# Performance work log

Hardware: AMD Instinct MI355X
Metric: run time of the kernel (lower is better)

Reference implementation:

```python
import jax, jax.numpy as jnp
import numpy as np

DECAY = 0.999
EPS = 1e-05


def setup_inputs() -> dict:
    key = jax.random.key(0)
    k1, k2 = jax.random.split(key)
    B, L, S, D, E = 32, 8, 512, 256, 2048
    x = jax.random.normal(k1, (B, L, S, D), dtype=jnp.float32)
    # stacked per-quantizer codebooks: embed[l] is the [dim, n_embed] buffer of Quantize l
    embed = jax.random.normal(k2, (L, D, E), dtype=jnp.float32)
    cluster_size = jnp.zeros((L, E), dtype=jnp.float32)
    embed_avg = embed.copy()
    return {"x": x, "embed": embed, "cluster_size": cluster_size, "embed_avg": embed_avg}


def reference(x, embed, cluster_size, embed_avg):
    # x: [B, L, S, D]; embed: [L, D, E]; cluster_size: [L, E]; embed_avg: [L, D, E]
    B, L, S, D = x.shape
    E = embed.shape[-1]

    dist = ((x * x).sum(-1, keepdims=True)
            - 2.0 * jnp.einsum('blsd,lde->blse', x, embed)
            + (embed * embed).sum(1)[None, :, None, :])
    ids = jnp.argmin(dist, axis=-1)  # argmax of -dist == argmin of dist; [B, L, S]

    # codebook lookup: embed_t[l, ids[b,l,s]] -> [B, L, S, D]
    embed_t = jnp.swapaxes(embed, 1, 2)  # [L, E, D]
    q = embed_t[jnp.arange(L)[None, :, None], ids]

    # EMA buffer updates (training mode; done on .data in torch, i.e. no grad)
    l_idx = jnp.broadcast_to(jnp.arange(L)[None, :, None], (B, L, S))
    counts = jnp.zeros((L, E), x.dtype).at[l_idx, ids].add(1.0)  # onehot.sum(0) per quantizer
    embed_sum = jnp.zeros((L, E, D), x.dtype).at[l_idx, ids].add(jax.lax.stop_gradient(x))
    embed_sum = jnp.swapaxes(embed_sum, 1, 2)  # [L, D, E] == flatten.T @ onehot
    new_cluster_size = DECAY * cluster_size + (1.0 - DECAY) * counts
    new_embed_avg = DECAY * embed_avg + (1.0 - DECAY) * embed_sum
    n = new_cluster_size.sum(-1, keepdims=True)  # [L, 1]
    cs = (new_cluster_size + EPS) / (n + E * EPS) * n
    new_embed = new_embed_avg / cs[:, None, :]

    # NOTE: the original loop overwrites `diff` each iteration then does `diff += diff`,
    # so the returned diff is 2 * diff_of_last_quantizer / length (faithfully reproduced).
    diff_last = jnp.mean((jax.lax.stop_gradient(q[:, L - 1]) - x[:, L - 1]) ** 2)
    diff = 2.0 * diff_last / L

    # straight-through estimator
    out = x + jax.lax.stop_gradient(q - x)
    return out, diff, ids, new_embed, new_cluster_size, new_embed_avg
```

## Files before the change

kernel.cpp:

```cpp
#include <hip/hip_runtime.h>

#define LL 8
#define BB 32
#define SS 512
#define DD 256
#define EE 2048
#define LED (LL*DD*EE)
#define LE  (LL*EE)
#define NROWS (BB*LL*SS)
#define NSEG 32

typedef __bf16 bf16x8 __attribute__((ext_vector_type(8)));
typedef float  f32x16 __attribute__((ext_vector_type(16)));

__global__ void prep_transpose_kernel(const float* __restrict__ embed,
                                      float* __restrict__ embed_t,
                                      float* __restrict__ norms,
                                      __bf16* __restrict__ frag) {
    __shared__ float tile[32][33];
    const int l  = blockIdx.z;
    const int d0 = blockIdx.y * 32;
    const int e0 = blockIdx.x * 32;
    const int tx = threadIdx.x, ty = threadIdx.y;

    float v = embed[((size_t)l*DD + d0 + ty)*EE + e0 + tx];
    tile[ty][tx] = v;
    __syncthreads();

    embed_t[((size_t)l*EE + e0 + ty)*DD + d0 + tx] = tile[tx][ty];

    const int t    = ty*32 + tx;
    const int ksl  = t >> 9;
    const int pos  = t & 511;
    const int lane = pos >> 3, j = pos & 7;
    const int klocal = (lane >> 5)*8 + j;
    const int e_loc  = lane & 31;
    float val = tile[ksl*16 + klocal][e_loc];
    __bf16 h = (__bf16)val;
    const int m  = blockIdx.x;
    const int ks = (d0 >> 4) + ksl;
    size_t segbase = (((size_t)(l*64 + m))*NSEG + 2*ks)*512 + pos;
    frag[segbase]       = h;
    frag[segbase + 512] = (__bf16)(val - (float)h);

    if (ty == 0) {
        float s = 0.f;
        #pragma unroll
        for (int i = 0; i < 32; ++i) s += tile[i][tx]*tile[i][tx];
        atomicAdd(&norms[l*EE + e0 + tx], s);
    }
}

__global__ __launch_bounds__(256, 2)
void argmin_mfma(const float* __restrict__ x,
                 const __bf16* __restrict__ frag,
                 const float* __restrict__ embed_t,
                 const float* __restrict__ norms,
                 int* __restrict__ ids_out,
                 int* __restrict__ counts_i,
                 float* __restrict__ out,
                 float* __restrict__ diff_acc) {
    __shared__ __bf16 slots[2][NSEG*512];
    __shared__ float  normbuf[EE];

    const int tid  = threadIdx.x;
    const int wave = tid >> 6, lane = tid & 63;
    const int l    = blockIdx.x & 7;
    const int rb   = blockIdx.x >> 3;
    const int idx  = rb*4 + wave;
    const int b    = idx >> 4, st = idx & 15;
    const int rowtile = (b*LL + l)*16 + st;

    {
        const float* np = norms + l*EE;
        for (int i = wave; i < 8; i += 4) {
            __builtin_amdgcn_global_load_lds(
                (const __attribute__((address_space(1))) void*)(np + i*256 + lane*4),
                (__attribute__((address_space(3))) void*)(normbuf + i*256), 16, 0, 0);
        }
    }

    bf16x8 bh[16], bl[16];
    {
        const float* xr = x + (size_t)(rowtile*32 + (lane & 31))*DD + (lane >> 5)*8;
        #pragma unroll
        for (int ks = 0; ks < 16; ++ks) {
            float4 v0 = *(const float4*)(xr + ks*16);
            float4 v1 = *(const float4*)(xr + ks*16 + 4);
            float f[8] = {v0.x, v0.y, v0.z, v0.w, v1.x, v1.y, v1.z, v1.w};
            #pragma unroll
            for (int j = 0; j < 8; ++j) {
                __bf16 h = (__bf16)f[j];
                bh[ks][j] = h;
                bl[ks][j] = (__bf16)(f[j] - (float)h);
            }
        }
    }

    const __bf16* fl = frag + (size_t)l*64*NSEG*512;

    auto stage = [&](int m, int buf) {
        const __bf16* src = fl + (size_t)m*NSEG*512 + lane*8;
        __bf16* dst = &slots[buf][0];
        for (int i = wave; i < NSEG; i += 4) {
            __builtin_amdgcn_global_load_lds(
                (const __attribute__((address_space(1))) void*)(src + i*512),
                (__attribute__((address_space(3))) void*)(dst + i*512), 16, 0, 0);
        }
    };

    float maxv = -3.4e38f;
    int   maxi = 0;

    stage(0, 0);
    __syncthreads();

    #pragma unroll 1
    for (int m = 0; m < 64; ++m) {
        const int buf = m & 1;
        if (m < 63) stage(m + 1, buf ^ 1);

        f32x16 a0, a1, a2;
        #pragma unroll
        for (int i = 0; i < 16; ++i) { a0[i] = 0.0f; a1[i] = 0.0f; a2[i] = 0.0f; }

        const __bf16* sA = &slots[buf][0];
        __builtin_amdgcn_s_setprio(1);
        #pragma unroll
        for (int k = 0; k < 16; ++k) {
            bf16x8 ah = *(const bf16x8*)(sA + (2*k    )*512 + lane*8);
            bf16x8 al = *(const bf16x8*)(sA + (2*k + 1)*512 + lane*8);
            a0 = __builtin_amdgcn_mfma_f32_32x32x16_bf16(ah, bh[k], a0, 0, 0, 0);
            a1 = __builtin_amdgcn_mfma_f32_32x32x16_bf16(ah, bl[k], a1, 0, 0, 0);
            a2 = __builtin_amdgcn_mfma_f32_32x32x16_bf16(al, bh[k], a2, 0, 0, 0);
        }
        __builtin_amdgcn_s_setprio(0);

        const int ebase = m*32 + 4*(lane >> 5);
        #pragma unroll
        for (int j = 0; j < 4; ++j) {
            float4 nv = *(const float4*)(normbuf + m*32 + 8*j + 4*(lane >> 5));
            #pragma unroll
            for (int rr = 0; rr < 4; ++rr) {
                float v = a0[4*j + rr] + a1[4*j + rr] + a2[4*j + rr];
                v = fmaf(-0.5f, (&nv.x)[rr], v);
                int e = ebase + rr + 8*j;
                if (v > maxv) { maxv = v; maxi = e; }
            }
        }
        __syncthreads();
    }

    float ov = __shfl_xor(maxv, 32, 64);
    int   oi = __shfl_xor(maxi, 32, 64);
    if (ov > maxv || (ov == maxv && oi < maxi)) { maxv = ov; maxi = oi; }
    if (lane < 32) {
        ids_out[(size_t)rowtile*32 + lane] = maxi;
        atomicAdd(&counts_i[l*EE + maxi], 1);
    }

    const float4* et4  = (const float4*)embed_t;
    const float4* x4   = (const float4*)x;
    float4*       out4 = (float4*)out;
    float sq = 0.f;
    #pragma unroll 4
    for (int r = 0; r < 32; ++r) {
        int id = __shfl(maxi, r);
        float4 qv = et4[((size_t)l*EE + id)*64 + lane];
        size_t o = ((size_t)rowtile*32 + r)*64 + lane;
        out4[o] = qv;
        if (l == LL - 1) {
            float4 xv = x4[o];
            float dx = qv.x - xv.x, dy = qv.y - xv.y, dz = qv.z - xv.z, dw = qv.w - xv.w;
            sq += dx*dx + dy*dy + dz*dz + dw*dw;
        }
    }
    if (l == LL - 1) {
        #pragma unroll
        for (int off = 32; off; off >>= 1) sq += __shfl_down(sq, off);
        if (lane == 0) atomicAdd(diff_acc, sq);
    }
}

__global__ __launch_bounds__(256)
void scan_kernel(const int* __restrict__ counts_i,
                 const float* __restrict__ cs_in,
                 int* __restrict__ bin_start,
                 int* __restrict__ cursor,
                 float* __restrict__ ncs_out,
                 float* __restrict__ n_out) {
    __shared__ int part[256];
    __shared__ float red[4];
    const int l = blockIdx.x, tid = threadIdx.x;
    const int base = l*EE + tid*8;
    int local[8], tsum = 0;
    float fsum = 0.f;
    #pragma unroll
    for (int j = 0; j < 8; ++j) {
        local[j] = counts_i[base + j];
        tsum += local[j];
        float v = 0.999f*cs_in[base + j] + 0.001f*(float)local[j];
        ncs_out[base + j] = v;
        fsum += v;
    }
    part[tid] = tsum;
    __syncthreads();
    for (int off = 1; off < 256; off <<= 1) {
        int v = (tid >= off) ? part[tid - off] : 0;
        __syncthreads();
        part[tid] += v;
        __syncthreads();
    }
    int run = part[tid] - tsum;
    #pragma unroll
    for (int j = 0; j < 8; ++j) {
        bin_start[base + j] = run;
        cursor[base + j]    = run;
        run += local[j];
    }
    #pragma unroll
    for (int off = 32; off; off >>= 1) fsum += __shfl_down(fsum, off);
    if ((tid & 63) == 0) red[tid >> 6] = fsum;
    __syncthreads();
    if (tid == 0) n_out[l] = red[0] + red[1] + red[2] + red[3];
}

__global__ __launch_bounds__(256)
void scatter_idx_kernel(const int* __restrict__ ids,
                        int* __restrict__ cursor,
                        int* __restrict__ sorted_rows) {
    const int r = blockIdx.x*256 + threadIdx.x;
    const int l = (r >> 9) & 7;
    const int e = ids[r];
    int pos = atomicAdd(&cursor[l*EE + e], 1);
    sorted_rows[l*(NROWS/LL) + pos] = r;
}

__global__ __launch_bounds__(256)
void segsum_kernel(const float* __restrict__ x,
                   const int* __restrict__ sorted_rows,
                   const int* __restrict__ bin_start,
                   const int* __restrict__ counts_i,
                   float* __restrict__ embed_sum) {
    const int bid = blockIdx.x;
    const int l   = bid >> 11;
    const int e   = bid & 2047;
    const int tid = threadIdx.x;
    const int start = bin_start[l*EE + e];
    const int cnt   = counts_i[l*EE + e];
    const int* rows = sorted_rows + l*(NROWS/LL);

    float acc = 0.f;
    int i = 0;
    for (; i + 1 < cnt; i += 2) {
        int r0 = rows[start + i], r1 = rows[start + i + 1];
        acc += x[(size_t)r0*DD + tid] + x[(size_t)r1*DD + tid];
    }
    if (i < cnt) acc += x[(size_t)rows[start + i]*DD + tid];
    embed_sum[((size_t)l*EE + e)*DD + tid] = acc;
}

__global__ void finalize_embed_kernel(const float* __restrict__ embed_avg,
                                      const float* __restrict__ embed_sum,
                                      const float* __restrict__ ncs,
                                      const float* __restrict__ n,
                                      float* __restrict__ nea_out,
                                      float* __restrict__ ne_out) {
    __shared__ float tile[32][33];
    const int l  = blockIdx.z;
    const int d0 = blockIdx.y * 32;
    const int e0 = blockIdx.x * 32;
    const int tx = threadIdx.x, ty = threadIdx.y;

    tile[ty][tx] = embed_sum[((size_t)l*EE + e0 + ty)*DD + d0 + tx];
    __syncthreads();
    const size_t idx = ((size_t)l*DD + d0 + ty)*EE + e0 + tx;
    float nea = 0.999f*embed_avg[idx] + 0.001f*tile[tx][ty];
    nea_out[idx] = nea;
    float nl = n[l];
    float c  = ncs[l*EE + e0 + tx];
    float cs = (c + 1e-5f) / (nl + 0.02048f) * nl;
    ne_out[idx] = nea / cs;
}

__global__ void diff_scale_kernel(const float* __restrict__ diff_acc,
                                  float* __restrict__ diff_out) {
    *diff_out = (*diff_acc / (float)(BB*SS*DD)) * 0.25f;
}

extern "C" void kernel_launch(void* const* d_in, const int* in_sizes, int n_in,
                              void* d_out, int out_size, void* d_ws, size_t ws_size,
                              hipStream_t stream) {
    const float* x            = (const float*)d_in[0];
    const float* embed        = (const float*)d_in[1];
    const float* cluster_size = (const float*)d_in[2];
    const float* embed_avg    = (const float*)d_in[3];

    float* out      = (float*)d_out;
    float* diff_out = out + 33554432;
    int*   ids_out  = (int*)(out + 33554433);
    float* ne_out   = out + 33685505;
    float* ncs_out  = out + 37879809;
    float* nea_out  = out + 37896193;

    float* ws        = (float*)d_ws;
    float* embed_t   = ws;
    float* embed_sum = ws + LED;
    int*   counts_i  = (int*)(ws + 2*(size_t)LED);
    float* norms     = ws + 2*(size_t)LED + LE;
    float* diff_acc  = norms + LE;
    float* n_ws      = diff_acc + 1;
    int*   bin_start = (int*)(n_ws + LL);
    int*   cursor    = bin_start + LE;
    int*   sorted_rows = cursor + LE;
    __bf16* embfrag  = (__bf16*)(sorted_rows + NROWS + 16);

    hipMemsetAsync(counts_i, 0, (size_t)(2*LE + 1) * sizeof(float), stream);

    prep_transpose_kernel<<<dim3(EE/32, DD/32, LL), dim3(32, 32), 0, stream>>>(
        embed, embed_t, norms, embfrag);

    argmin_mfma<<<1024, 256, 0, stream>>>(x, embfrag, embed_t, norms, ids_out,
                                          counts_i, out, diff_acc);

    scan_kernel<<<LL, 256, 0, stream>>>(counts_i, cluster_size, bin_start, cursor,
                                        ncs_out, n_ws);

    scatter_idx_kernel<<<NROWS/256, 256, 0, stream>>>(ids_out, cursor, sorted_rows);

    segsum_kernel<<<LE, 256, 0, stream>>>(x, sorted_rows, bin_start, counts_i, embed_sum);

    finalize_embed_kernel<<<dim3(EE/32, DD/32, LL), dim3(32, 32), 0, stream>>>(
        embed_avg, embed_sum, ncs_out, n_ws, nea_out, ne_out);

    diff_scale_kernel<<<1, 1, 0, stream>>>(diff_acc, diff_out);
}
```

Before: 959.7 us.

## Fold codebook norms into MFMA and software-pipeline argmin epilogue

Adds a 33rd fragment segment holding -0.5*|e|^2 split into bf16 hi/lo, paired with a constant-ones B fragment, so the norm bias is accumulated by one extra MFMA instead of a separate LDS norm buffer and FMA. The main loop is restructured to ping-pong accumulators so the argmin compare for the previous codebook tile is interleaved with the current tile's MFMAs, using sched_group_barrier hints and register prefetch of A fragments. Accumulators are merged from three to two. It adds a small kernel launch and extra LDS and register pressure, and the bf16 split of the norm may change rounding slightly.

```diff
diff --git a/kernel.cpp b/kernel.cpp
--- a/kernel.cpp
+++ b/kernel.cpp
@@ -8,7 +8,7 @@
 #define LED (LL*DD*EE)
 #define LE  (LL*EE)
 #define NROWS (BB*LL*SS)
-#define NSEG 32
+#define NSEG 33
 
 typedef __bf16 bf16x8 __attribute__((ext_vector_type(8)));
 typedef float  f32x16 __attribute__((ext_vector_type(16)));
@@ -51,17 +51,31 @@
     }
 }
 
+__global__ void norm_seg_kernel(const float* __restrict__ norms,
+                                __bf16* __restrict__ frag) {
+    const int bid  = blockIdx.x;
+    const int lane = threadIdx.x;
+    bf16x8 v;
+    #pragma unroll
+    for (int j = 0; j < 8; ++j) v[j] = (__bf16)0.0f;
+    if (lane < 32) {
+        float nv = -0.5f * norms[(bid >> 6)*EE + (bid & 63)*32 + lane];
+        __bf16 h = (__bf16)nv;
+        v[0] = h;
+        v[1] = (__bf16)(nv - (float)h);
+    }
+    *(bf16x8*)(frag + ((size_t)bid*NSEG + 32)*512 + lane*8) = v;
+}
+
 __global__ __launch_bounds__(256, 2)
 void argmin_mfma(const float* __restrict__ x,
                  const __bf16* __restrict__ frag,
                  const float* __restrict__ embed_t,
-                 const float* __restrict__ norms,
                  int* __restrict__ ids_out,
                  int* __restrict__ counts_i,
                  float* __restrict__ out,
                  float* __restrict__ diff_acc) {
     __shared__ __bf16 slots[2][NSEG*512];
-    __shared__ float  normbuf[EE];
 
     const int tid  = threadIdx.x;
     const int wave = tid >> 6, lane = tid & 63;
@@ -71,16 +85,7 @@
     const int b    = idx >> 4, st = idx & 15;
     const int rowtile = (b*LL + l)*16 + st;
 
-    {
-        const float* np = norms + l*EE;
-        for (int i = wave; i < 8; i += 4) {
-            __builtin_amdgcn_global_load_lds(
-                (const __attribute__((address_space(1))) void*)(np + i*256 + lane*4),
-                (__attribute__((address_space(3))) void*)(normbuf + i*256), 16, 0, 0);
-        }
-    }
-
-    bf16x8 bh[16], bl[16];
+    bf16x8 bh[17], bl[16];
     {
         const float* xr = x + (size_t)(rowtile*32 + (lane & 31))*DD + (lane >> 5)*8;
         #pragma unroll
@@ -95,6 +100,9 @@
                 bl[ks][j] = (__bf16)(f[j] - (float)h);
             }
         }
+        #pragma unroll
+        for (int j = 0; j < 8; ++j) bh[16][j] = (__bf16)0.0f;
+        if (lane < 32) { bh[16][0] = (__bf16)1.0f; bh[16][1] = (__bf16)1.0f; }
     }
 
     const __bf16* fl = frag + (size_t)l*64*NSEG*512;
@@ -109,46 +117,66 @@
         }
     };
 
-    float maxv = -3.4e38f;
+    float maxv = -1e30f;
     int   maxi = 0;
 
-    stage(0, 0);
-    __syncthreads();
-
-    #pragma unroll 1
-    for (int m = 0; m < 64; ++m) {
-        const int buf = m & 1;
-        if (m < 63) stage(m + 1, buf ^ 1);
-
-        f32x16 a0, a1, a2;
-        #pragma unroll
-        for (int i = 0; i < 16; ++i) { a0[i] = 0.0f; a1[i] = 0.0f; a2[i] = 0.0f; }
-
-        const __bf16* sA = &slots[buf][0];
-        __builtin_amdgcn_s_setprio(1);
+    auto step = [&](int m, f32x16& Pc, f32x16& Qc, f32x16& Pp, f32x16& Qp) {
+        #pragma unroll
+        for (int i = 0; i < 16; ++i) { Pc[i] = 0.0f; Qc[i] = 0.0f; }
+        if (m < 63) stage(m + 1, (m & 1) ^ 1);
+        const __bf16* sA = &slots[m & 1][0];
+        const int pbase = (m - 1)*32 + 4*(lane >> 5);
+
+        bf16x8 ah = *(const bf16x8*)(sA + 0*512 + lane*8);
+        bf16x8 al = *(const bf16x8*)(sA + 1*512 + lane*8);
         #pragma unroll
         for (int k = 0; k < 16; ++k) {
-            bf16x8 ah = *(const bf16x8*)(sA + (2*k    )*512 + lane*8);
-            bf16x8 al = *(const bf16x8*)(sA + (2*k + 1)*512 + lane*8);
-            a0 = __builtin_amdgcn_mfma_f32_32x32x16_bf16(ah, bh[k], a0, 0, 0, 0);
-            a1 = __builtin_amdgcn_mfma_f32_32x32x16_bf16(ah, bl[k], a1, 0, 0, 0);
-            a2 = __builtin_amdgcn_mfma_f32_32x32x16_bf16(al, bh[k], a2, 0, 0, 0);
-        }
-        __builtin_amdgcn_s_setprio(0);
-
-        const int ebase = m*32 + 4*(lane >> 5);
-        #pragma unroll
-        for (int j = 0; j < 4; ++j) {
-            float4 nv = *(const float4*)(normbuf + m*32 + 8*j + 4*(lane >> 5));
-            #pragma unroll
-            for (int rr = 0; rr < 4; ++rr) {
-                float v = a0[4*j + rr] + a1[4*j + rr] + a2[4*j + rr];
-                v = fmaf(-0.5f, (&nv.x)[rr], v);
-                int e = ebase + rr + 8*j;
+            bf16x8 nh, nl;
+            if (k < 15) {
+                nh = *(const bf16x8*)(sA + (2*k + 2)*512 + lane*8);
+                nl = *(const bf16x8*)(sA + (2*k + 3)*512 + lane*8);
+            } else {
+                nh = *(const bf16x8*)(sA + 32*512 + lane*8);
+                nl = nh;
+            }
+            Pc = __builtin_amdgcn_mfma_f32_32x32x16_bf16(ah, bh[k], Pc, 0, 0, 0);
+            Qc = __builtin_amdgcn_mfma_f32_32x32x16_bf16(ah, bl[k], Qc, 0, 0, 0);
+            Pc = __builtin_amdgcn_mfma_f32_32x32x16_bf16(al, bh[k], Pc, 0, 0, 0);
+            {
+                float v = Pp[k] + Qp[k];
+                int e = pbase + (k & 3) + 8*(k >> 2);
                 if (v > maxv) { maxv = v; maxi = e; }
             }
-        }
+            ah = nh; al = nl;
+            if (k < 15) __builtin_amdgcn_sched_group_barrier(0x100, 2, 0);
+            else        __builtin_amdgcn_sched_group_barrier(0x100, 1, 0);
+            __builtin_amdgcn_sched_group_barrier(0x008, 3, 0);
+            __builtin_amdgcn_sched_group_barrier(0x002, 8, 0);
+        }
+        Pc = __builtin_amdgcn_mfma_f32_32x32x16_bf16(ah, bh[16], Pc, 0, 0, 0);
         __syncthreads();
+    };
+
+    f32x16 PA, QA, PB, QB;
+    #pragma unroll
+    for (int i = 0; i < 16; ++i) { PB[i] = -1e30f; QB[i] = -1e30f; }
+
+    stage(0, 0);
+    __syncthreads();
+
+    #pragma unroll 1
+    for (int t = 0; t < 32; ++t) {
+        step(2*t,     PA, QA, PB, QB);
+        step(2*t + 1, PB, QB, PA, QA);
+    }
+    {
+        const int pbase = 63*32 + 4*(lane >> 5);
+        #pragma unroll
+        for (int k = 0; k < 16; ++k) {
+            float v = PB[k] + QB[k];
+            int e = pbase + (k & 3) + 8*(k >> 2);
+            if (v > maxv) { maxv = v; maxi = e; }
+        }
     }
 
     float ov = __shfl_xor(maxv, 32, 64);
@@ -320,7 +348,9 @@
     prep_transpose_kernel<<<dim3(EE/32, DD/32, LL), dim3(32, 32), 0, stream>>>(
         embed, embed_t, norms, embfrag);
 
-    argmin_mfma<<<1024, 256, 0, stream>>>(x, embfrag, embed_t, norms, ids_out,
+    norm_seg_kernel<<<LL*64, 64, 0, stream>>>(norms, embfrag);
+
+    argmin_mfma<<<1024, 256, 0, stream>>>(x, embfrag, embed_t, ids_out,
                                           counts_i, out, diff_acc);
 
     scan_kernel<<<LL, 256, 0, stream>>>(counts_i, cluster_size, bin_start, cursor,
```

Measured after the change: 945.0 us. No clear change (-1.5%).
